# Kernel optimization log

Measured on AMD Instinct MI355X. Metric: run time of the kernel, lower is better.

## Reference

```python
import jax, jax.numpy as jnp
import numpy as np

N = 100000   # num_nodes
E = 100000   # events in current batch
D = 128      # memory_dim
RAW = 128    # raw_msg_dim
T = 128      # time_dim
MSG = 2 * D + RAW + T  # IdentityMessage out_channels = 512


def setup_inputs() -> dict:
    key = jax.random.key(0)
    ks = jax.random.split(key, 12)
    s = 1.0 / np.sqrt(D)
    return {
        "memory": jax.random.normal(ks[0], (N, D), jnp.float32),
        "last_update": jnp.zeros((N,), jnp.int32),
        "src": jax.random.randint(ks[1], (E,), 0, N, jnp.int32),
        "dst": jax.random.randint(ks[2], (E,), 0, N, jnp.int32),
        "t": jax.random.randint(ks[3], (E,), 0, 1000000, jnp.int32),
        "raw_msg": jax.random.normal(ks[4], (E, RAW), jnp.float32),
        "time_w": jax.random.normal(ks[5], (T,), jnp.float32),
        "time_b": jax.random.normal(ks[6], (T,), jnp.float32),
        "w_ih": jax.random.uniform(ks[7], (3 * D, MSG), jnp.float32, -s, s),
        "w_hh": jax.random.uniform(ks[8], (3 * D, D), jnp.float32, -s, s),
        "b_ih": jax.random.uniform(ks[9], (3 * D,), jnp.float32, -s, s),
        "b_hh": jax.random.uniform(ks[10], (3 * D,), jnp.float32, -s, s),
    }


def reference(memory, last_update, src, dst, t, raw_msg,
              time_w, time_b, w_ih, w_hh, b_ih, b_hh):
    n_nodes, d = memory.shape
    dtype = memory.dtype

    def time_enc(t_rel):  # Time2Vec: cos(Linear(1 -> time_dim))
        return jnp.cos(t_rel[:, None] * time_w + time_b)

    # source-store messages: node key == src, roles (src, dst)
    enc_s = time_enc((t - last_update[src]).astype(dtype))
    msg_s = jnp.concatenate([memory[src], memory[dst], raw_msg, enc_s], axis=1)
    # destination-store messages: node key == dst, roles swapped
    enc_d = time_enc((t - last_update[dst]).astype(dtype))
    msg_d = jnp.concatenate([memory[dst], memory[src], raw_msg, enc_d], axis=1)

    idx = jnp.concatenate([src, dst])          # [2E] destination node of each message
    msg = jnp.concatenate([msg_s, msg_d], 0)   # [2E, MSG]
    tt = jnp.concatenate([t, t])               # [2E]

    # scatter-mean aggregation per node (empty nodes -> 0)
    sums = jax.ops.segment_sum(msg, idx, num_segments=n_nodes)
    cnt = jax.ops.segment_sum(jnp.ones((idx.shape[0],), dtype), idx, num_segments=n_nodes)
    aggr = sums / jnp.maximum(cnt, 1.0)[:, None]

    # GRUCell(aggr, memory)
    gx = aggr @ w_ih.T + b_ih
    gh = memory @ w_hh.T + b_hh
    xr, xz, xn = jnp.split(gx, 3, axis=1)
    hr, hz, hn = jnp.split(gh, 3, axis=1)
    r = jax.nn.sigmoid(xr + hr)
    z = jax.nn.sigmoid(xz + hz)
    n = jnp.tanh(xn + r * hn)
    new_memory = (1.0 - z) * n + z * memory

    # scatter-max of event times; empty nodes -> 0 (matches zero-init scatter)
    new_last_update = jnp.maximum(
        jax.ops.segment_max(tt, idx, num_segments=n_nodes), 0)

    return new_memory, new_last_update
```

## Files before the change

### kernel.cpp

```cpp
#include <hip/hip_runtime.h>

#define N_NODES 100000
#define N_EVENTS 100000
#define D 128
#define KTOT 640
#define NP 512
#define BM 64

#define OFF_AGGR 0
#define OFF_CNT  76800000
#define OFF_LAST (OFF_CNT  + N_NODES * 4)
#define OFF_OFFS (OFF_LAST + N_NODES * 4)
#define OFF_CUR  (OFF_OFFS + N_NODES * 4)
#define OFF_CSR  (OFF_CUR  + N_NODES * 4)
#define OFF_BP   (OFF_CSR  + 2 * N_EVENTS * 16)
#define OFF_PART (OFF_BP   + NP * KTOT * 2)

#define SCAN_BLOCKS 98

typedef __attribute__((ext_vector_type(8))) short bf16x8;
typedef __attribute__((ext_vector_type(4))) float f32x4;

__device__ __forceinline__ short f2bf(float x) {
    unsigned u = __float_as_uint(x);
    u = (u + 0x7FFFu + ((u >> 16) & 1u)) >> 16;
    return (short)u;
}

#define BAR() do { asm volatile("s_waitcnt lgkmcnt(0)" ::: "memory"); \
                   __builtin_amdgcn_s_barrier(); } while (0)

__global__ __launch_bounds__(256) void k_init(unsigned* __restrict__ cnt,
                                              int* __restrict__ lastmax,
                                              const float* __restrict__ wih,
                                              const float* __restrict__ whh,
                                              short* __restrict__ bp) {
    int i = blockIdx.x * blockDim.x + threadIdx.x;
    int stride = gridDim.x * blockDim.x;
    for (int j = i; j < N_NODES; j += stride) { cnt[j] = 0u; lastmax[j] = 0; }
    for (int j = i; j < NP * KTOT; j += stride) {
        int n = j / KTOT, k = j - n * KTOT;
        float v = 0.f;
        if (n < 384) {
            if (k < 512) v = wih[n * 512 + k];
            else if (n < 256) v = whh[n * 128 + (k - 512)];
        } else if (k >= 512) {
            v = whh[(n - 128) * 128 + (k - 512)];
        }
        bp[j] = f2bf(v);
    }
}

__global__ __launch_bounds__(256) void k_count(const int* __restrict__ src,
                                               const int* __restrict__ dst,
                                               const int* __restrict__ t,
                                               unsigned* __restrict__ cnt,
                                               int* __restrict__ lastmax) {
    int e = blockIdx.x * blockDim.x + threadIdx.x;
    if (e < N_EVENTS) {
        int s = src[e], d = dst[e], te = t[e];
        atomicAdd(&cnt[s], 1u);
        atomicAdd(&cnt[d], 1u);
        atomicMax(&lastmax[s], te);
        atomicMax(&lastmax[d], te);
    }
}

__global__ __launch_bounds__(256) void k_scanA(const unsigned* __restrict__ cnt,
                                               int* __restrict__ partial) {
    const int b = blockIdx.x, tid = threadIdx.x;
    const int base = b * 1024 + tid * 4;
    int s = 0;
    if (base + 3 < N_NODES) {
        int4 c = *(const int4*)((const int*)cnt + base);
        s = c.x + c.y + c.z + c.w;
    } else {
        for (int k = 0; k < 4; ++k)
            if (base + k < N_NODES) s += (int)cnt[base + k];
    }
#pragma unroll
    for (int off = 32; off; off >>= 1) s += __shfl_down(s, off, 64);
    __shared__ int ws[4];
    if ((tid & 63) == 0) ws[tid >> 6] = s;
    __syncthreads();
    if (tid == 0) partial[b] = ws[0] + ws[1] + ws[2] + ws[3];
}

__global__ __launch_bounds__(128) void k_scanB(int* __restrict__ partial) {
    __shared__ int p[128];
    const int tid = threadIdx.x;
    p[tid] = (tid < SCAN_BLOCKS) ? partial[tid] : 0;
    __syncthreads();
    if (tid == 0) {
        int run = 0;
        for (int i = 0; i < SCAN_BLOCKS; ++i) { int v = p[i]; p[i] = run; run += v; }
    }
    __syncthreads();
    if (tid < SCAN_BLOCKS) partial[tid] = p[tid];
}

__global__ __launch_bounds__(256) void k_scanC(const unsigned* __restrict__ cnt,
                                               const int* __restrict__ partial,
                                               int* __restrict__ offs,
                                               int* __restrict__ cursor,
                                               const int* __restrict__ lastmax,
                                               float* __restrict__ outLast) {
    __shared__ int sums[256];
    const int b = blockIdx.x, tid = threadIdx.x;
    const int base = b * 1024 + tid * 4;
    int c0 = 0, c1 = 0, c2 = 0, c3 = 0;
    if (base + 3 < N_NODES) {
        int4 c = *(const int4*)((const int*)cnt + base);
        c0 = c.x; c1 = c.y; c2 = c.z; c3 = c.w;
    } else {
        if (base     < N_NODES) c0 = (int)cnt[base];
        if (base + 1 < N_NODES) c1 = (int)cnt[base + 1];
        if (base + 2 < N_NODES) c2 = (int)cnt[base + 2];
        if (base + 3 < N_NODES) c3 = (int)cnt[base + 3];
    }
    sums[tid] = c0 + c1 + c2 + c3;
    __syncthreads();
    for (int off = 1; off < 256; off <<= 1) {
        int v = (tid >= off) ? sums[tid - off] : 0;
        __syncthreads();
        sums[tid] += v;
        __syncthreads();
    }
    int run = partial[b] + (tid > 0 ? sums[tid - 1] : 0);
    const int o0 = run, o1 = o0 + c0, o2 = o1 + c1, o3 = o2 + c2;
    if (base + 3 < N_NODES) {
        *(int4*)(offs + base)   = make_int4(o0, o1, o2, o3);
        *(int4*)(cursor + base) = make_int4(o0, o1, o2, o3);
        int4 lm = *(const int4*)(lastmax + base);
        float4 lo = make_float4((float)lm.x, (float)lm.y, (float)lm.z, (float)lm.w);
        *(float4*)(outLast + base) = lo;
    } else {
        if (base     < N_NODES) { offs[base]     = o0; cursor[base]     = o0; outLast[base]     = (float)lastmax[base]; }
        if (base + 1 < N_NODES) { offs[base + 1] = o1; cursor[base + 1] = o1; outLast[base + 1] = (float)lastmax[base + 1]; }
        if (base + 2 < N_NODES) { offs[base + 2] = o2; cursor[base + 2] = o2; outLast[base + 2] = (float)lastmax[base + 2]; }
        if (base + 3 < N_NODES) { offs[base + 3] = o3; cursor[base + 3] = o3; outLast[base + 3] = (float)lastmax[base + 3]; }
    }
}

__global__ __launch_bounds__(256) void k_fill(const int* __restrict__ src,
                                              const int* __restrict__ dst,
                                              const int* __restrict__ t,
                                              int* __restrict__ cursor,
                                              int4* __restrict__ csr) {
    int e = blockIdx.x * blockDim.x + threadIdx.x;
    if (e < N_EVENTS) {
        int s = src[e], d = dst[e], te = t[e];
        int ps = atomicAdd(&cursor[s], 1);
        csr[ps] = make_int4(d, te, e, 0);
        int pd = atomicAdd(&cursor[d], 1);
        csr[pd] = make_int4(s, te, e, 0);
    }
}

__global__ __launch_bounds__(128) void k_aggr(const float* __restrict__ mem,
                                              const float* __restrict__ raw,
                                              const int* __restrict__ lu,
                                              const float* __restrict__ tw,
                                              const float* __restrict__ tb,
                                              const int* __restrict__ offs,
                                              const unsigned* __restrict__ cnt,
                                              const int4* __restrict__ csr,
                                              unsigned short* __restrict__ aggr) {
    const int node = blockIdx.x;
    const int i = threadIdx.x;
    const unsigned deg = cnt[node];
    float a0 = 0.f, a1 = 0.f, a2 = 0.f;
    if (deg) {
        const int start = offs[node];
        const int lun = lu[node];
        const float wi = tw[i], bi = tb[i];
        for (unsigned j = 0; j < deg; ++j) {
            int4 rec = csr[start + j];
            const int other = rec.x, te = rec.y, e = rec.z;
            a0 += mem[other * D + i];
            a1 += raw[e * D + i];
            const float tr = (float)(te - lun);
            a2 += cosf(__fadd_rn(__fmul_rn(tr, wi), bi));
        }
        const float inv = 1.f / (float)deg;
        a0 *= inv; a1 *= inv; a2 *= inv;
    }
    aggr[node * 384 + i]       = (unsigned short)f2bf(a0);
    aggr[node * 384 + 128 + i] = (unsigned short)f2bf(a1);
    aggr[node * 384 + 256 + i] = (unsigned short)f2bf(a2);
}

template<int C>
__device__ __forceinline__ void ld_chunk(const float* __restrict__ mem,
                                         const unsigned short* __restrict__ aggr,
                                         int nc, int cg,
                                         float4& f0, float4& f1, bf16x8& av) {
    if constexpr (C >= 2 && C < 8) {
        av = *(const bf16x8*)(aggr + nc * 384 + (C - 2) * 64 + cg * 8);
    } else {
        constexpr int kc = (C < 2) ? C * 64 : (C - 8) * 64;
        const float4* p = (const float4*)(mem + nc * D + kc + cg * 8);
        f0 = p[0];
        f1 = p[1];
    }
}

template<int C>
__device__ __forceinline__ void wr_chunk(short* __restrict__ buf, int row, int cg,
                                         float scale01,
                                         const float4& f0, const float4& f1,
                                         const bf16x8& av) {
    bf16x8 h;
    if constexpr (C >= 2 && C < 8) {
        h = av;
    } else {
        const float s = (C < 2) ? scale01 : 1.f;
        h[0] = f2bf(f0.x * s); h[1] = f2bf(f0.y * s);
        h[2] = f2bf(f0.z * s); h[3] = f2bf(f0.w * s);
        h[4] = f2bf(f1.x * s); h[5] = f2bf(f1.y * s);
        h[6] = f2bf(f1.z * s); h[7] = f2bf(f1.w * s);
    }
    *(bf16x8*)((char*)buf + row * 128 + ((cg * 16) ^ ((row & 7) << 4))) = h;
}

__device__ __forceinline__ void mfma_chunk(const short* __restrict__ sAbuf,
                                           int lr, int lk, int swz,
                                           const short* __restrict__ bR,
                                           const short* __restrict__ bZ,
                                           const short* __restrict__ bN, int kk0,
                                           f32x4* accR, f32x4* accZ, f32x4* accN) {
#pragma unroll
    for (int k2 = 0; k2 < 2; ++k2) {
        bf16x8 a[4];
#pragma unroll
        for (int mt = 0; mt < 4; ++mt)
            a[mt] = *(const bf16x8*)((const char*)sAbuf + (mt * 16 + lr) * 128 +
                                     ((k2 * 64 + lk * 16) ^ swz));
        const int kk = kk0 + k2 * 32;
        bf16x8 fR = *(const bf16x8*)(bR + kk);
        bf16x8 fZ = *(const bf16x8*)(bZ + kk);
        bf16x8 fN = *(const bf16x8*)(bN + kk);
#pragma unroll
        for (int mt = 0; mt < 4; ++mt) {
            accR[mt] = __builtin_amdgcn_mfma_f32_16x16x32_bf16(a[mt], fR, accR[mt], 0, 0, 0);
            accZ[mt] = __builtin_amdgcn_mfma_f32_16x16x32_bf16(a[mt], fZ, accZ[mt], 0, 0, 0);
            accN[mt] = __builtin_amdgcn_mfma_f32_16x16x32_bf16(a[mt], fN, accN[mt], 0, 0, 0);
        }
    }
}

__global__ __launch_bounds__(512, 4) void k_gemm_gru(const float* __restrict__ mem,
                                                     const unsigned short* __restrict__ aggr,
                                                     const unsigned* __restrict__ cnt,
                                                     const short* __restrict__ bp,
                                                     const float* __restrict__ bih,
                                                     const float* __restrict__ bhh,
                                                     float* __restrict__ out) {
    __shared__ short sA[3][BM * 64];
    const int tid = threadIdx.x;
    const int node0 = blockIdx.x * BM;
    const int row_ = tid >> 3;
    const int cg = tid & 7;
    const int nodeS = node0 + row_;
    const int ncS = nodeS < N_NODES ? nodeS : N_NODES - 1;

    const int l = tid & 63, w = tid >> 6;
    const int lr = l & 15, lk = l >> 4;
    const int swz = (lr & 7) << 4;

    float4 fA0, fA1, fB0, fB1;
    bf16x8 aA, aB;

    const float scale01 = (cnt[ncS] > 0u) ? 1.f : 0.f;
    ld_chunk<0>(mem, aggr, ncS, cg, fA0, fA1, aA);
    ld_chunk<1>(mem, aggr, ncS, cg, fB0, fB1, aB);
    ld_chunk<2>(mem, aggr, ncS, cg, fA0, fA1, aA);
    ld_chunk<3>(mem, aggr, ncS, cg, fB0, fB1, aB);

    f32x4 accR[4], accZ[4], accNx[4], accNh[4];
#pragma unroll
    for (int mt = 0; mt < 4; ++mt) {
        accR[mt]  = (f32x4){0.f, 0.f, 0.f, 0.f};
        accZ[mt]  = (f32x4){0.f, 0.f, 0.f, 0.f};
        accNx[mt] = (f32x4){0.f, 0.f, 0.f, 0.f};
        accNh[mt] = (f32x4){0.f, 0.f, 0.f, 0.f};
    }

    const short* bR = bp + (w * 16 + lr) * KTOT + lk * 8;
    const short* bZ = bp + ((8 + w) * 16 + lr) * KTOT + lk * 8;
    const short* bX = bp + ((16 + w) * 16 + lr) * KTOT + lk * 8;
    const short* bH = bp + ((24 + w) * 16 + lr) * KTOT + lk * 8;

    wr_chunk<0>(sA[0], row_, cg, scale01, fA0, fA1, aA);
    wr_chunk<1>(sA[1], row_, cg, scale01, fB0, fB1, aB);
    BAR();

    mfma_chunk(sA[0], lr, lk, swz, bR, bZ, bX, 0,   accR, accZ, accNx);
    wr_chunk<2>(sA[2], row_, cg, scale01, fA0, fA1, aA);
    ld_chunk<4>(mem, aggr, ncS, cg, fA0, fA1, aA);
    BAR();
    mfma_chunk(sA[1], lr, lk, swz, bR, bZ, bX, 64,  accR, accZ, accNx);
    wr_chunk<3>(sA[0], row_, cg, scale01, fB0, fB1, aB);
    ld_chunk<5>(mem, aggr, ncS, cg, fB0, fB1, aB);
    BAR();
    mfma_chunk(sA[2], lr, lk, swz, bR, bZ, bX, 128, accR, accZ, accNx);
    wr_chunk<4>(sA[1], row_, cg, scale01, fA0, fA1, aA);
    ld_chunk<6>(mem, aggr, ncS, cg, fA0, fA1, aA);
    BAR();
    mfma_chunk(sA[0], lr, lk, swz, bR, bZ, bX, 192, accR, accZ, accNx);
    wr_chunk<5>(sA[2], row_, cg, scale01, fB0, fB1, aB);
    ld_chunk<7>(mem, aggr, ncS, cg, fB0, fB1, aB);
    BAR();
    mfma_chunk(sA[1], lr, lk, swz, bR, bZ, bX, 256, accR, accZ, accNx);
    wr_chunk<6>(sA[0], row_, cg, scale01, fA0, fA1, aA);
    ld_chunk<8>(mem, aggr, ncS, cg, fA0, fA1, aA);
    BAR();
    mfma_chunk(sA[2], lr, lk, swz, bR, bZ, bX, 320, accR, accZ, accNx);
    wr_chunk<7>(sA[1], row_, cg, scale01, fB0, fB1, aB);
    ld_chunk<9>(mem, aggr, ncS, cg, fB0, fB1, aB);
    BAR();
    mfma_chunk(sA[0], lr, lk, swz, bR, bZ, bX, 384, accR, accZ, accNx);
    wr_chunk<8>(sA[2], row_, cg, scale01, fA0, fA1, aA);
    BAR();
    mfma_chunk(sA[1], lr, lk, swz, bR, bZ, bX, 448, accR, accZ, accNx);
    wr_chunk<9>(sA[0], row_, cg, scale01, fB0, fB1, aB);
    BAR();
    mfma_chunk(sA[2], lr, lk, swz, bR, bZ, bH, 512, accR, accZ, accNh);
    mfma_chunk(sA[0], lr, lk, swz, bR, bZ, bH, 576, accR, accZ, accNh);

    const int jcol = w * 16 + lr;
    const float br  = bih[jcol]       + bhh[jcol];
    const float bz  = bih[128 + jcol] + bhh[128 + jcol];
    const float bxn = bih[256 + jcol];
    const float bhn = bhh[256 + jcol];
#pragma unroll
    for (int mt = 0; mt < 4; ++mt) {
#pragma unroll
        for (int i = 0; i < 4; ++i) {
            const int node = node0 + mt * 16 + lk * 4 + i;
            if (node < N_NODES) {
                const float rp = accR[mt][i] + br;
                const float zp = accZ[mt][i] + bz;
                const float xn = accNx[mt][i] + bxn;
                const float hn = accNh[mt][i] + bhn;
                const float rg = 1.f / (1.f + expf(-rp));
                const float zg = 1.f / (1.f + expf(-zp));
                const float ng = tanhf(xn + rg * hn);
                const float mo = mem[node * D + jcol];
                out[node * D + jcol] = (1.f - zg) * ng + zg * mo;
            }
        }
    }
}

extern "C" void kernel_launch(void* const* d_in, const int* in_sizes, int n_in,
                              void* d_out, int out_size, void* d_ws, size_t ws_size,
                              hipStream_t stream) {
    const float* memory      = (const float*)d_in[0];
    const int*   last_update = (const int*)d_in[1];
    const int*   src         = (const int*)d_in[2];
    const int*   dst         = (const int*)d_in[3];
    const int*   t           = (const int*)d_in[4];
    const float* raw_msg     = (const float*)d_in[5];
    const float* time_w      = (const float*)d_in[6];
    const float* time_b      = (const float*)d_in[7];
    const float* w_ih        = (const float*)d_in[8];
    const float* w_hh        = (const float*)d_in[9];
    const float* b_ih        = (const float*)d_in[10];
    const float* b_hh        = (const float*)d_in[11];

    float* out = (float*)d_out;
    char* ws = (char*)d_ws;
    unsigned short* aggr  = (unsigned short*)(ws + OFF_AGGR);
    unsigned* cnt         = (unsigned*)(ws + OFF_CNT);
    int*      lastmax     = (int*)(ws + OFF_LAST);
    int*      offs        = (int*)(ws + OFF_OFFS);
    int*      cursor      = (int*)(ws + OFF_CUR);
    int4*     csr         = (int4*)(ws + OFF_CSR);
    short*    bpw         = (short*)(ws + OFF_BP);
    int*      partial     = (int*)(ws + OFF_PART);

    k_init<<<512, 256, 0, stream>>>(cnt, lastmax, w_ih, w_hh, bpw);
    k_count<<<(N_EVENTS + 255) / 256, 256, 0, stream>>>(src, dst, t, cnt, lastmax);
    k_scanA<<<SCAN_BLOCKS, 256, 0, stream>>>(cnt, partial);
    k_scanB<<<1, 128, 0, stream>>>(partial);
    k_scanC<<<SCAN_BLOCKS, 256, 0, stream>>>(cnt, partial, offs, cursor,
                                             lastmax, out + N_NODES * D);
    k_fill<<<(N_EVENTS + 255) / 256, 256, 0, stream>>>(src, dst, t, cursor, csr);
    k_aggr<<<N_NODES, 128, 0, stream>>>(memory, raw_msg, last_update, time_w, time_b,
                                        offs, cnt, csr, aggr);
    k_gemm_gru<<<(N_NODES + BM - 1) / BM, 512, 0, stream>>>(memory, aggr, cnt, bpw,
                                                            b_ih, b_hh, out);
}
```

Before: 255.9 us.

## Load GEMM A operands directly from global into registers, dropping LDS staging

Result: slower. 383.6 us (+49.9%).

```diff
diff --git a/kernel.cpp b/kernel.cpp
--- a/kernel.cpp
+++ b/kernel.cpp
@@ -27,8 +27,12 @@
     return (short)u;
 }
 
-#define BAR() do { asm volatile("s_waitcnt lgkmcnt(0)" ::: "memory"); \
-                   __builtin_amdgcn_s_barrier(); } while (0)
+__device__ __forceinline__ bf16x8 cvt8(const float4& x0, const float4& x1) {
+    bf16x8 h;
+    h[0] = f2bf(x0.x); h[1] = f2bf(x0.y); h[2] = f2bf(x0.z); h[3] = f2bf(x0.w);
+    h[4] = f2bf(x1.x); h[5] = f2bf(x1.y); h[6] = f2bf(x1.z); h[7] = f2bf(x1.w);
+    return h;
+}
 
 __global__ __launch_bounds__(256) void k_init(unsigned* __restrict__ cnt,
                                               int* __restrict__ lastmax,
@@ -190,92 +194,89 @@
     aggr[node * 384 + 256 + i] = (unsigned short)f2bf(a2);
 }
 
-template<int C>
-__device__ __forceinline__ void ld_chunk(const float* __restrict__ mem,
-                                         const unsigned short* __restrict__ aggr,
-                                         int nc, int cg,
-                                         float4& f0, float4& f1, bf16x8& av) {
-    if constexpr (C >= 2 && C < 8) {
-        av = *(const bf16x8*)(aggr + nc * 384 + (C - 2) * 64 + cg * 8);
-    } else {
-        constexpr int kc = (C < 2) ? C * 64 : (C - 8) * 64;
-        const float4* p = (const float4*)(mem + nc * D + kc + cg * 8);
-        f0 = p[0];
-        f1 = p[1];
-    }
-}
-
-template<int C>
-__device__ __forceinline__ void wr_chunk(short* __restrict__ buf, int row, int cg,
-                                         float scale01,
-                                         const float4& f0, const float4& f1,
-                                         const bf16x8& av) {
-    bf16x8 h;
-    if constexpr (C >= 2 && C < 8) {
-        h = av;
-    } else {
-        const float s = (C < 2) ? scale01 : 1.f;
-        h[0] = f2bf(f0.x * s); h[1] = f2bf(f0.y * s);
-        h[2] = f2bf(f0.z * s); h[3] = f2bf(f0.w * s);
-        h[4] = f2bf(f1.x * s); h[5] = f2bf(f1.y * s);
-        h[6] = f2bf(f1.z * s); h[7] = f2bf(f1.w * s);
-    }
-    *(bf16x8*)((char*)buf + row * 128 + ((cg * 16) ^ ((row & 7) << 4))) = h;
-}
-
-__device__ __forceinline__ void mfma_chunk(const short* __restrict__ sAbuf,
-                                           int lr, int lk, int swz,
-                                           const short* __restrict__ bR,
-                                           const short* __restrict__ bZ,
-                                           const short* __restrict__ bN, int kk0,
-                                           f32x4* accR, f32x4* accZ, f32x4* accN) {
+
+#define MFMA(a, b, c) __builtin_amdgcn_mfma_f32_16x16x32_bf16(a, b, c, 0, 0, 0)
+
+template<int CM>
+__device__ __forceinline__ void do_mem_chunk(const float* __restrict__ mem,
+                                             const int* nc, const unsigned* msk,
+                                             const short* __restrict__ bR,
+                                             const short* __restrict__ bZ,
+                                             const short* __restrict__ bX,
+                                             const short* __restrict__ bH,
+                                             int lk,
+                                             f32x4* accR, f32x4* accZ,
+                                             f32x4* accNx, f32x4* accNh) {
 #pragma unroll
     for (int k2 = 0; k2 < 2; ++k2) {
-        bf16x8 a[4];
-#pragma unroll
-        for (int mt = 0; mt < 4; ++mt)
-            a[mt] = *(const bf16x8*)((const char*)sAbuf + (mt * 16 + lr) * 128 +
-                                     ((k2 * 64 + lk * 16) ^ swz));
-        const int kk = kk0 + k2 * 32;
+        const int kk = CM * 64 + k2 * 32;
+        bf16x8 fR0 = *(const bf16x8*)(bR + kk);
+        bf16x8 fZ0 = *(const bf16x8*)(bZ + kk);
+        bf16x8 fX  = *(const bf16x8*)(bX + kk);
+        bf16x8 fR1 = *(const bf16x8*)(bR + 512 + kk);
+        bf16x8 fZ1 = *(const bf16x8*)(bZ + 512 + kk);
+        bf16x8 fH  = *(const bf16x8*)(bH + 512 + kk);
+        const bf16x8 zero = {};
+#pragma unroll
+        for (int mt = 0; mt < 4; ++mt) {
+            const float4* p = (const float4*)(mem + nc[mt] * D + kk + lk * 8);
+            const float4 x0 = p[0], x1 = p[1];
+            const bf16x8 au = cvt8(x0, x1);
+            const bf16x8 as = msk[mt] ? au : zero;
+            accR[mt]  = MFMA(au, fR1, accR[mt]);
+            accZ[mt]  = MFMA(au, fZ1, accZ[mt]);
+            accNh[mt] = MFMA(au, fH,  accNh[mt]);
+            accR[mt]  = MFMA(as, fR0, accR[mt]);
+            accZ[mt]  = MFMA(as, fZ0, accZ[mt]);
+            accNx[mt] = MFMA(as, fX,  accNx[mt]);
+        }
+    }
+}
+
+template<int CA>
+__device__ __forceinline__ void do_aggr_chunk(const unsigned short* __restrict__ aggr,
+                                              const int* nc,
+                                              const short* __restrict__ bR,
+                                              const short* __restrict__ bZ,
+                                              const short* __restrict__ bX,
+                                              int lk,
+                                              f32x4* accR, f32x4* accZ, f32x4* accNx) {
+#pragma unroll
+    for (int k2 = 0; k2 < 2; ++k2) {
+        const int kk = 128 + CA * 64 + k2 * 32;
         bf16x8 fR = *(const bf16x8*)(bR + kk);
         bf16x8 fZ = *(const bf16x8*)(bZ + kk);
-        bf16x8 fN = *(const bf16x8*)(bN + kk);
+        bf16x8 fX = *(const bf16x8*)(bX + kk);
 #pragma unroll
         for (int mt = 0; mt < 4; ++mt) {
-            accR[mt] = __builtin_amdgcn_mfma_f32_16x16x32_bf16(a[mt], fR, accR[mt], 0, 0, 0);
-            accZ[mt] = __builtin_amdgcn_mfma_f32_16x16x32_bf16(a[mt], fZ, accZ[mt], 0, 0, 0);
-            accN[mt] = __builtin_amdgcn_mfma_f32_16x16x32_bf16(a[mt], fN, accN[mt], 0, 0, 0);
-        }
-    }
-}
-
-__global__ __launch_bounds__(512, 4) void k_gemm_gru(const float* __restrict__ mem,
+            bf16x8 a = *(const bf16x8*)(aggr + nc[mt] * 384 + CA * 64 + k2 * 32 + lk * 8);
+            accR[mt]  = MFMA(a, fR, accR[mt]);
+            accZ[mt]  = MFMA(a, fZ, accZ[mt]);
+            accNx[mt] = MFMA(a, fX, accNx[mt]);
+        }
+    }
+}
+
+__global__ __launch_bounds__(512, 2) void k_gemm_gru(const float* __restrict__ mem,
                                                      const unsigned short* __restrict__ aggr,
                                                      const unsigned* __restrict__ cnt,
                                                      const short* __restrict__ bp,
                                                      const float* __restrict__ bih,
                                                      const float* __restrict__ bhh,
                                                      float* __restrict__ out) {
-    __shared__ short sA[3][BM * 64];
     const int tid = threadIdx.x;
     const int node0 = blockIdx.x * BM;
-    const int row_ = tid >> 3;
-    const int cg = tid & 7;
-    const int nodeS = node0 + row_;
-    const int ncS = nodeS < N_NODES ? nodeS : N_NODES - 1;
-
     const int l = tid & 63, w = tid >> 6;
     const int lr = l & 15, lk = l >> 4;
-    const int swz = (lr & 7) << 4;
-
-    float4 fA0, fA1, fB0, fB1;
-    bf16x8 aA, aB;
-
-    const float scale01 = (cnt[ncS] > 0u) ? 1.f : 0.f;
-    ld_chunk<0>(mem, aggr, ncS, cg, fA0, fA1, aA);
-    ld_chunk<1>(mem, aggr, ncS, cg, fB0, fB1, aB);
-    ld_chunk<2>(mem, aggr, ncS, cg, fA0, fA1, aA);
-    ld_chunk<3>(mem, aggr, ncS, cg, fB0, fB1, aB);
+
+    int nc[4];
+    unsigned msk[4];
+#pragma unroll
+    for (int mt = 0; mt < 4; ++mt) {
+        const int node = node0 + mt * 16 + lr;
+        nc[mt] = node < N_NODES ? node : N_NODES - 1;
+        msk[mt] = cnt[nc[mt]];
+    }
 
     f32x4 accR[4], accZ[4], accNx[4], accNh[4];
 #pragma unroll
@@ -291,42 +292,14 @@
     const short* bX = bp + ((16 + w) * 16 + lr) * KTOT + lk * 8;
     const short* bH = bp + ((24 + w) * 16 + lr) * KTOT + lk * 8;
 
-    wr_chunk<0>(sA[0], row_, cg, scale01, fA0, fA1, aA);
-    wr_chunk<1>(sA[1], row_, cg, scale01, fB0, fB1, aB);
-    BAR();
-
-    mfma_chunk(sA[0], lr, lk, swz, bR, bZ, bX, 0,   accR, accZ, accNx);
-    wr_chunk<2>(sA[2], row_, cg, scale01, fA0, fA1, aA);
-    ld_chunk<4>(mem, aggr, ncS, cg, fA0, fA1, aA);
-    BAR();
-    mfma_chunk(sA[1], lr, lk, swz, bR, bZ, bX, 64,  accR, accZ, accNx);
-    wr_chunk<3>(sA[0], row_, cg, scale01, fB0, fB1, aB);
-    ld_chunk<5>(mem, aggr, ncS, cg, fB0, fB1, aB);
-    BAR();
-    mfma_chunk(sA[2], lr, lk, swz, bR, bZ, bX, 128, accR, accZ, accNx);
-    wr_chunk<4>(sA[1], row_, cg, scale01, fA0, fA1, aA);
-    ld_chunk<6>(mem, aggr, ncS, cg, fA0, fA1, aA);
-    BAR();
-    mfma_chunk(sA[0], lr, lk, swz, bR, bZ, bX, 192, accR, accZ, accNx);
-    wr_chunk<5>(sA[2], row_, cg, scale01, fB0, fB1, aB);
-    ld_chunk<7>(mem, aggr, ncS, cg, fB0, fB1, aB);
-    BAR();
-    mfma_chunk(sA[1], lr, lk, swz, bR, bZ, bX, 256, accR, accZ, accNx);
-    wr_chunk<6>(sA[0], row_, cg, scale01, fA0, fA1, aA);
-    ld_chunk<8>(mem, aggr, ncS, cg, fA0, fA1, aA);
-    BAR();
-    mfma_chunk(sA[2], lr, lk, swz, bR, bZ, bX, 320, accR, accZ, accNx);
-    wr_chunk<7>(sA[1], row_, cg, scale01, fB0, fB1, aB);
-    ld_chunk<9>(mem, aggr, ncS, cg, fB0, fB1, aB);
-    BAR();
-    mfma_chunk(sA[0], lr, lk, swz, bR, bZ, bX, 384, accR, accZ, accNx);
-    wr_chunk<8>(sA[2], row_, cg, scale01, fA0, fA1, aA);
-    BAR();
-    mfma_chunk(sA[1], lr, lk, swz, bR, bZ, bX, 448, accR, accZ, accNx);
-    wr_chunk<9>(sA[0], row_, cg, scale01, fB0, fB1, aB);
-    BAR();
-    mfma_chunk(sA[2], lr, lk, swz, bR, bZ, bH, 512, accR, accZ, accNh);
-    mfma_chunk(sA[0], lr, lk, swz, bR, bZ, bH, 576, accR, accZ, accNh);
+    do_mem_chunk<0>(mem, nc, msk, bR, bZ, bX, bH, lk, accR, accZ, accNx, accNh);
+    do_aggr_chunk<0>(aggr, nc, bR, bZ, bX, lk, accR, accZ, accNx);
+    do_aggr_chunk<1>(aggr, nc, bR, bZ, bX, lk, accR, accZ, accNx);
+    do_aggr_chunk<2>(aggr, nc, bR, bZ, bX, lk, accR, accZ, accNx);
+    do_mem_chunk<1>(mem, nc, msk, bR, bZ, bX, bH, lk, accR, accZ, accNx, accNh);
+    do_aggr_chunk<3>(aggr, nc, bR, bZ, bX, lk, accR, accZ, accNx);
+    do_aggr_chunk<4>(aggr, nc, bR, bZ, bX, lk, accR, accZ, accNx);
+    do_aggr_chunk<5>(aggr, nc, bR, bZ, bX, lk, accR, accZ, accNx);
 
     const int jcol = w * 16 + lr;
     const float br  = bih[jcol]       + bhh[jcol];
```
